# Performance work log

Measured on AMD Instinct MI355X. Metric: run time of the kernel, lower is better.

The kernel has to match this reference:

```python
import jax, jax.numpy as jnp
import numpy as np

NUM_HEADS = 16
ROPE_BASE = 10000.0


def _rope_tables(head_dim, seq_len, dtype=jnp.float32):
    # Half-split convention: rotate first half against second half.
    inv_freq = 1.0 / (ROPE_BASE ** (jnp.arange(0, head_dim, 2, dtype=dtype) / head_dim))
    pos = jnp.arange(seq_len, dtype=dtype)
    angles_half = jnp.einsum('s,d->sd', pos, inv_freq)          # (S, D/2)
    angles = jnp.concatenate([angles_half, angles_half], -1)     # (S, D)
    return jnp.cos(angles), jnp.sin(angles)


def _apply_rope(x, cos, sin):
    # x: (H, S, D); cos/sin: (S, D) broadcast over heads
    half = x.shape[-1] // 2
    x1, x2 = x[..., :half], x[..., half:]
    x_rot = jnp.concatenate([-x2, x1], axis=-1)
    return x * cos + x_rot * sin


def setup_inputs() -> dict:
    key = jax.random.key(0)
    S, E = 2048, 2048
    ks = jax.random.split(key, 9)
    sc = 0.02
    return {
        'x': jax.random.normal(ks[0], (S, E), jnp.float32),
        'Wq': jax.random.normal(ks[1], (E, E), jnp.float32) * sc,
        'bq': jax.random.normal(ks[2], (E,), jnp.float32) * sc,
        'Wk': jax.random.normal(ks[3], (E, E), jnp.float32) * sc,
        'bk': jax.random.normal(ks[4], (E,), jnp.float32) * sc,
        'Wv': jax.random.normal(ks[5], (E, E), jnp.float32) * sc,
        'bv': jax.random.normal(ks[6], (E,), jnp.float32) * sc,
        'Wo': jax.random.normal(ks[7], (E, E), jnp.float32) * sc,
        'bo': jax.random.normal(ks[8], (E,), jnp.float32) * sc,
    }


def reference(x, Wq, bq, Wk, bk, Wv, bv, Wo, bo):
    S, E = x.shape
    H = NUM_HEADS
    D = E // H
    scale = D ** 0.5
    cos, sin = _rope_tables(D, S, x.dtype)

    def proj(W, b):
        return (x @ W.T + b).reshape(S, H, D).transpose(1, 0, 2)  # (H, S, D)

    q = _apply_rope(proj(Wq, bq), cos, sin)
    k = _apply_rope(proj(Wk, bk), cos, sin)
    v = proj(Wv, bv)

    scores = jnp.einsum('hsd,htd->hst', q, k) / scale  # (H, S, S)
    attn = jax.nn.softmax(scores, axis=-1)
    out = jnp.einsum('hst,htd->hsd', attn, v)          # (H, S, D)
    # Faithful to the original's transpose(0,1).view(S,E) on a (1,H,S,D)
    # tensor: an in-order (head-major) flatten reinterpreted as (S, E).
    out = out.reshape(S, E)
    return out @ Wo.T + bo
```

## Files before the change

### kernel.cpp

```cpp
#include <hip/hip_runtime.h>

#define SDIM 2048
#define EDIM 2048
#define NHEAD 16
#define DHEAD 128

typedef __attribute__((ext_vector_type(8))) short short8;
typedef __attribute__((ext_vector_type(4))) float floatx4;

__device__ __forceinline__ float bf2f(ushort u) {
    union { uint i; float f; } v; v.i = ((uint)u) << 16; return v.f;
}
__device__ __forceinline__ ushort f2bf(float f) {
    union { float f; uint i; } v; v.f = f;
    uint r = v.i + 0x7fff + ((v.i >> 16) & 1);
    return (ushort)(r >> 16);
}

__device__ __forceinline__ void gload_lds16(const ushort* g, ushort* l) {
    __builtin_amdgcn_global_load_lds(
        (const __attribute__((address_space(1))) void*)g,
        (__attribute__((address_space(3))) void*)l, 16, 0, 0);
}

__global__ void convert5_kernel(
    const float* __restrict__ s0, const float* __restrict__ s1,
    const float* __restrict__ s2, const float* __restrict__ s3,
    const float* __restrict__ s4,
    ushort* __restrict__ d0, ushort* __restrict__ d1,
    ushort* __restrict__ d2, ushort* __restrict__ d3,
    ushort* __restrict__ d4)
{
    const float* src; ushort* dst;
    switch (blockIdx.y) {
        case 0: src = s0; dst = d0; break;
        case 1: src = s1; dst = d1; break;
        case 2: src = s2; dst = d2; break;
        case 3: src = s3; dst = d3; break;
        default: src = s4; dst = d4; break;
    }
    int i = blockIdx.x * blockDim.x + threadIdx.x;
    float4 f = ((const float4*)src)[i];
    ushort4 o;
    o.x = f2bf(f.x); o.y = f2bf(f.y); o.z = f2bf(f.z); o.w = f2bf(f.w);
    ((ushort4*)dst)[i] = o;
}

#define QPRESCALE 0.12754245f

template <int MODE>
__global__ __launch_bounds__(512, 2) void gemm256(
    const ushort* __restrict__ A,
    const ushort* __restrict__ B0, const ushort* __restrict__ B1, const ushort* __restrict__ B2,
    const float* __restrict__ s0, const float* __restrict__ s1, const float* __restrict__ s2,
    ushort* __restrict__ C0, ushort* __restrict__ C1, ushort* __restrict__ Vtg,
    float* __restrict__ Cf)
{
    __shared__ __align__(16) ushort smem[2][2][2][128 * 64];

    const int tid  = threadIdx.x;
    const int lane = tid & 63;
    const int wave = tid >> 6;
    const int l15 = lane & 15, quad = lane >> 4, l7 = lane & 7;
    const int wm = wave & 1, wn = wave >> 1;
    const int bm = blockIdx.x * 256;

    int which = 0, ks = 0, n0, NT;
    const ushort* Abase;
    const ushort* Bsel;
    const float*  bia;
    if constexpr (MODE == 0) {
        which = blockIdx.y >> 3;
        n0 = (blockIdx.y & 7) * 256;
        NT = EDIM / 64;
        Abase = A;
        Bsel = (which == 0) ? B0 : (which == 1) ? B1 : B2;
        bia  = (which == 0) ? s0 : (which == 1) ? s1 : s2;
    } else {
        ks = blockIdx.y >> 3;
        n0 = (blockIdx.y & 7) * 256;
        NT = (EDIM / 2) / 64;
        Abase = A + ks * (EDIM / 2);
        Bsel  = B0 + ks * (EDIM / 2);
        bia   = s0;
    }

    const int srow = tid >> 3;
    const int sgc  = (((tid & 7) ^ ((tid >> 3) & 7)) << 3);

    floatx4 acc[8][4];
#pragma unroll
    for (int i = 0; i < 8; i++)
#pragma unroll
        for (int j = 0; j < 4; j++) acc[i][j] = (floatx4)0.0f;

    auto stageA = [&](int tile, int h) {
        const ushort* g = Abase + (size_t)(bm + h * 128 + srow) * EDIM + tile * 64 + sgc;
        ushort* l = &smem[tile & 1][0][h][0] + tid * 8;
        gload_lds16(g, l);
        gload_lds16(g + (size_t)64 * EDIM, l + 4096);
    };
    auto stageB = [&](int tile, int h) {
        const ushort* g = Bsel + (size_t)(n0 + h * 128 + srow) * EDIM + tile * 64 + sgc;
        ushort* l = &smem[tile & 1][1][h][0] + tid * 8;
        gload_lds16(g, l);
        gload_lds16(g + (size_t)64 * EDIM, l + 4096);
    };

    stageA(0, 0); stageA(0, 1); stageB(0, 0); stageB(0, 1);
    stageB(1, 0); stageB(1, 1);
    asm volatile("s_waitcnt vmcnt(4)" ::: "memory");
    __builtin_amdgcn_s_barrier();

    const int c0 = ((quad ^ l7) << 3);
    const int c1 = (((quad + 4) ^ l7) << 3);
    const int brow0 = (wn & 1) * 64;

    short8 af[4], b0[4], b1[4];

#define MFMA16(AOFF, AF, BF) \
    _Pragma("unroll") \
    for (int mf = 0; mf < 4; mf++) \
        _Pragma("unroll") \
        for (int an = 0; an < 4; an++) \
            acc[(AOFF) + mf][an] = __builtin_amdgcn_mfma_f32_16x16x32_bf16( \
                AF[mf], BF[an], acc[(AOFF) + mf][an], 0, 0, 0);

#define PH_PRE() do { \
    asm volatile("" ::: "memory"); \
    __builtin_amdgcn_s_barrier(); \
    asm volatile("s_waitcnt lgkmcnt(0)" ::: "memory"); \
    __builtin_amdgcn_sched_barrier(0); \
    __builtin_amdgcn_s_setprio(1); \
} while (0)
#define PH_POST() do { \
    __builtin_amdgcn_s_setprio(0); \
    asm volatile("" ::: "memory"); \
    __builtin_amdgcn_s_barrier(); \
} while (0)

    for (int t = 0; t < NT; ++t) {
        const ushort* aH = &smem[t & 1][0][wm][0];
        const ushort* bH = &smem[t & 1][1][wn >> 1][0];

#pragma unroll
        for (int mf = 0; mf < 4; mf++)
            af[mf] = *(const short8*)(aH + (mf * 16 + l15) * 64 + c0);
#pragma unroll
        for (int an = 0; an < 4; an++)
            b0[an] = *(const short8*)(bH + (brow0 + an * 16 + l15) * 64 + c0);
        if (t + 1 < NT) stageA(t + 1, 0);
        PH_PRE();
        MFMA16(0, af, b0);
        PH_POST();

        short8 ag[4];
#pragma unroll
        for (int mf = 0; mf < 4; mf++)
            ag[mf] = *(const short8*)(aH + (mf * 16 + l15) * 64 + c1);
#pragma unroll
        for (int an = 0; an < 4; an++)
            b1[an] = *(const short8*)(bH + (brow0 + an * 16 + l15) * 64 + c1);
        if (t + 1 < NT) stageA(t + 1, 1);
        PH_PRE();
        MFMA16(0, ag, b1);
        PH_POST();

#pragma unroll
        for (int mf = 0; mf < 4; mf++)
            af[mf] = *(const short8*)(aH + (64 + mf * 16 + l15) * 64 + c0);
        if (t + 2 < NT) stageB(t + 2, 0);
        PH_PRE();
        MFMA16(4, af, b0);
        PH_POST();

#pragma unroll
        for (int mf = 0; mf < 4; mf++)
            ag[mf] = *(const short8*)(aH + (64 + mf * 16 + l15) * 64 + c1);
        if (t + 2 < NT) stageB(t + 2, 1);
        asm volatile("" ::: "memory");
        __builtin_amdgcn_s_barrier();
        asm volatile("s_waitcnt lgkmcnt(0)" ::: "memory");
        __builtin_amdgcn_sched_barrier(0);
        __builtin_amdgcn_s_setprio(1);
        MFMA16(4, ag, b1);
        __builtin_amdgcn_s_setprio(0);
        if (t < NT - 2) asm volatile("s_waitcnt vmcnt(4)" ::: "memory");
        else            asm volatile("s_waitcnt vmcnt(0)" ::: "memory");
        __builtin_amdgcn_s_barrier();
    }
#undef MFMA16
#undef PH_PRE
#undef PH_POST

    if constexpr (MODE == 1) {
#pragma unroll
        for (int an = 0; an < 4; an++) {
            int col = n0 + wn * 64 + an * 16 + l15;
            float bv = (ks == 0) ? bia[col] : 0.0f;
#pragma unroll
            for (int am = 0; am < 8; am++) {
                int row = bm + wm * 128 + am * 16 + quad * 4;
#pragma unroll
                for (int r = 0; r < 4; r++)
                    atomicAdd(&Cf[(size_t)(row + r) * EDIM + col], acc[am][an][r] + bv);
            }
        }
        return;
    }

    if (which == 2) {
#pragma unroll
        for (int an = 0; an < 4; an++) {
            int col = n0 + wn * 64 + an * 16 + l15;
            int h = col >> 7, d = col & 127;
            float bv = bia[col];
            ushort* cp = Vtg + (size_t)h * SDIM * DHEAD + (size_t)d * SDIM;
#pragma unroll
            for (int am = 0; am < 8; am++) {
                int s = bm + wm * 128 + am * 16 + quad * 4;
                ushort4 pk;
                pk.x = f2bf(acc[am][an][0] + bv);
                pk.y = f2bf(acc[am][an][1] + bv);
                pk.z = f2bf(acc[am][an][2] + bv);
                pk.w = f2bf(acc[am][an][3] + bv);
                *(ushort4*)(cp + s) = pk;
            }
        }
    } else {
        ushort* C = (which == 0) ? C0 : C1;
        const float psc = (which == 0) ? QPRESCALE : 1.0f;
        float* xch = (float*)smem;
        float bv[4], invf[4];
#pragma unroll
        for (int an = 0; an < 4; an++) {
            bv[an]   = bia[n0 + wn * 64 + an * 16 + l15];
            invf[an] = __expf((float)(an * 16 + l15) * -0.14391157f);
        }
        const int mybase = wave * 1024 + quad * 16 + l15;
        const int pbase  = (wave ^ 2) * 1024 + quad * 16 + l15;
        const int rowb = bm + wm * 128 + quad * 4;
#pragma unroll
        for (int am2 = 0; am2 < 4; am2++) {
            __syncthreads();
#pragma unroll
            for (int sl = 0; sl < 2; sl++) {
                int am = am2 * 2 + sl;
#pragma unroll
                for (int an = 0; an < 4; an++)
#pragma unroll
                    for (int r = 0; r < 4; r++)
                        xch[sl * 8192 + mybase + an * 256 + r * 64] = acc[am][an][r] + bv[an];
            }
            __syncthreads();
#pragma unroll
            for (int sl = 0; sl < 2; sl++) {
                int am = am2 * 2 + sl;
#pragma unroll
                for (int an = 0; an < 4; an++) {
                    int col = n0 + wn * 64 + an * 16 + l15;
#pragma unroll
                    for (int r = 0; r < 4; r++) {
                        int row = rowb + am * 16 + r;
                        float v = acc[am][an][r] + bv[an];
                        float w = xch[sl * 8192 + pbase + an * 256 + r * 64];
                        float ang = (float)row * invf[an];
                        float rev = ang * 0.15915494309f;
                        rev -= floorf(rev);
                        float arad = rev * 6.28318530718f;
                        float sn = __sinf(arad), cs = __cosf(arad);
                        float o = ((wn & 1) == 0) ? (v * cs - w * sn) : (v * cs + w * sn);
                        C[(size_t)row * EDIM + col] = f2bf(o * psc);
                    }
                }
            }
        }
    }
}

template <typename OUTT, int KSPLIT>
__global__ __launch_bounds__(256) void gemm_bt(
    const ushort* __restrict__ A,
    const ushort* __restrict__ B0, const ushort* __restrict__ B1, const ushort* __restrict__ B2,
    const float* __restrict__ s0, const float* __restrict__ s1, const float* __restrict__ s2,
    OUTT* __restrict__ C0, OUTT* __restrict__ C1, OUTT* __restrict__ C2,
    int nbpm)
{
    __shared__ __align__(16) ushort smem[2 * 128 * 32];
    ushort* a_s = smem;
    ushort* b_s = smem + 128 * 32;

    const int tid = threadIdx.x;
    const int wave = tid >> 6, lane = tid & 63;
    const int l15 = lane & 15, quad = lane >> 4;
    const int wm = wave & 1, wn = wave >> 1;
    const int bm = blockIdx.x * 128;
    const int which = blockIdx.y / nbpm;
    const int n0 = (blockIdx.y % nbpm) * 128;

    const ushort* B;
    const float*  bia;
    OUTT*         C;
    const ushort* Abase;
    if constexpr (KSPLIT == 2) {
        B = B0; bia = s0; C = C0;
        Abase = A + which * (EDIM / 2);
    } else {
        B   = (which == 0) ? B0 : (which == 1) ? B1 : B2;
        bia = (which == 0) ? s0 : (which == 1) ? s1 : s2;
        C   = (which == 0) ? C0 : (which == 1) ? C1 : C2;
        Abase = A;
    }
    const ushort* Bbase = (KSPLIT == 2) ? B + which * (EDIM / 2) : B;

    floatx4 acc[4][4];
#pragma unroll
    for (int i = 0; i < 4; i++)
#pragma unroll
        for (int j = 0; j < 4; j++) acc[i][j] = (floatx4)0.0f;

    const int t1 = tid + 256;
    const int row0 = tid >> 2, kc0 = (tid & 3) * 8;
    const int row1 = t1 >> 2,  kc1 = (t1 & 3) * 8;

    for (int k0 = 0; k0 < EDIM / KSPLIT; k0 += 32) {
        __syncthreads();
        gload_lds16(Abase + (size_t)(bm + row0) * EDIM + k0 + kc0, a_s + tid * 8);
        gload_lds16(Abase + (size_t)(bm + row1) * EDIM + k0 + kc1, a_s + t1 * 8);
        gload_lds16(Bbase + (size_t)(n0 + row0) * EDIM + k0 + kc0, b_s + tid * 8);
        gload_lds16(Bbase + (size_t)(n0 + row1) * EDIM + k0 + kc1, b_s + t1 * 8);
        __syncthreads();

        short8 af[4], bf[4];
#pragma unroll
        for (int mt = 0; mt < 4; mt++)
            af[mt] = *(const short8*)(a_s + (wm * 64 + mt * 16 + l15) * 32 + quad * 8);
#pragma unroll
        for (int nt = 0; nt < 4; nt++)
            bf[nt] = *(const short8*)(b_s + (wn * 64 + nt * 16 + l15) * 32 + quad * 8);
#pragma unroll
        for (int mt = 0; mt < 4; mt++)
#pragma unroll
            for (int nt = 0; nt < 4; nt++)
                acc[mt][nt] = __builtin_amdgcn_mfma_f32_16x16x32_bf16(af[mt], bf[nt], acc[mt][nt], 0, 0, 0);
    }

    if constexpr (KSPLIT == 2) {
#pragma unroll
        for (int nt = 0; nt < 4; nt++) {
            int col = n0 + wn * 64 + nt * 16 + l15;
            float bv = (which == 0) ? bia[col] : 0.0f;
#pragma unroll
            for (int mt = 0; mt < 4; mt++) {
#pragma unroll
                for (int r = 0; r < 4; r++) {
                    int row = bm + wm * 64 + mt * 16 + quad * 4 + r;
                    atomicAdd(&((float*)C)[(size_t)row * EDIM + col], acc[mt][nt][r] + bv);
                }
            }
        }
    } else {
#pragma unroll
        for (int nt = 0; nt < 4; nt++) {
            int col = n0 + wn * 64 + nt * 16 + l15;
            float bv = bia[col];
#pragma unroll
            for (int mt = 0; mt < 4; mt++) {
#pragma unroll
                for (int r = 0; r < 4; r++) {
                    int row = bm + wm * 64 + mt * 16 + quad * 4 + r;
                    float v = acc[mt][nt][r] + bv;
                    if constexpr (sizeof(OUTT) == 2)
                        ((ushort*)C)[(size_t)row * EDIM + col] = f2bf(v);
                    else
                        ((float*)C)[(size_t)row * EDIM + col] = v;
                }
            }
        }
    }
}

#define MFIX2 17.31234049f
__global__ __launch_bounds__(256, 4) void attn_kernel(
    const ushort* __restrict__ Q, const ushort* __restrict__ K,
    const ushort* __restrict__ Vtg,
    ushort* __restrict__ Opart, float* __restrict__ Lsum,
    ushort* __restrict__ Ab, int nsplit)
{
    __shared__ __align__(16) ushort Ks[64 * 128];
    __shared__ __align__(16) ushort Vt[128 * 64];
    __shared__ __align__(16) ushort Ps[64 * 64];

    const int bid = blockIdx.x;
    const int head = bid & 15, qt = (bid >> 4) & 31, half = bid >> 9;
    const int tid = threadIdx.x, wave = tid >> 6, lane = tid & 63;
    const int l15 = lane & 15, quad = lane >> 4;
    const int l7 = l15 & 7;
    const int kstart = half * (SDIM / nsplit);
    const int ntile = (SDIM / nsplit) / 64;

    short8 qf[4];
    {
        int s = qt * 64 + wave * 16 + l15;
        const ushort* qp = Q + (size_t)s * EDIM + head * DHEAD;
#pragma unroll
        for (int kc = 0; kc < 4; kc++) qf[kc] = *(const short8*)(qp + kc * 32 + quad * 8);
    }

    floatx4 o[8];
#pragma unroll
    for (int i = 0; i < 8; i++) o[i] = (floatx4)0.0f;
    float lsum = 0.0f;

    const int krow = tid >> 4, kc8 = tid & 15;
    const int vd = tid >> 3, vc8 = tid & 7;
    const int prow = wave * 16 + l15;

    for (int kv = 0; kv < ntile; kv++) {
        const int k0 = kstart + kv * 64;
        __syncthreads();
#pragma unroll
        for (int i = 0; i < 4; i++) {
            int row = krow + i * 16;
            uint4 v = *(const uint4*)(K + (size_t)(k0 + row) * EDIM + head * DHEAD + kc8 * 8);
            *(uint4*)(Ks + row * 128 + ((kc8 ^ (row & 7)) << 3)) = v;
        }
#pragma unroll
        for (int i = 0; i < 4; i++) {
            int d = vd + i * 32;
            uint4 v = *(const uint4*)(Vtg + (size_t)head * SDIM * DHEAD + (size_t)d * SDIM + k0 + vc8 * 8);
            *(uint4*)(Vt + d * 64 + ((vc8 ^ (d & 7)) << 3)) = v;
        }
        __syncthreads();

#pragma unroll
        for (int nt = 0; nt < 4; nt++) {
            floatx4 st = (floatx4)0.0f;
#pragma unroll
            for (int kc = 0; kc < 4; kc++) {
                short8 kfr = *(const short8*)(Ks + (nt * 16 + l15) * 128 + (((kc * 4 + quad) ^ l7) << 3));
                st = __builtin_amdgcn_mfma_f32_16x16x32_bf16(kfr, qf[kc], st, 0, 0, 0);
            }
            ushort4 pk;
            float p0 = __builtin_amdgcn_exp2f(st[0] - MFIX2);
            float p1 = __builtin_amdgcn_exp2f(st[1] - MFIX2);
            float p2 = __builtin_amdgcn_exp2f(st[2] - MFIX2);
            float p3 = __builtin_amdgcn_exp2f(st[3] - MFIX2);
            lsum += (p0 + p1) + (p2 + p3);
            pk.x = f2bf(p0); pk.y = f2bf(p1); pk.z = f2bf(p2); pk.w = f2bf(p3);
            int c2 = (nt * 2 + (quad >> 1)) ^ l7;
            *(ushort4*)(Ps + prow * 64 + (c2 << 3) + ((quad & 1) << 2)) = pk;
        }

#pragma unroll
        for (int kc2 = 0; kc2 < 2; kc2++) {
            short8 af = *(const short8*)(Ps + prow * 64 + (((kc2 * 4 + quad) ^ l7) << 3));
#pragma unroll
            for (int nt2 = 0; nt2 < 8; nt2++) {
                short8 bfr = *(const short8*)(Vt + (nt2 * 16 + l15) * 64 + (((kc2 * 4 + quad) ^ l7) << 3));
                o[nt2] = __builtin_amdgcn_mfma_f32_16x16x32_bf16(af, bfr, o[nt2], 0, 0, 0);
            }
        }
    }

    lsum += __shfl_xor(lsum, 16);
    lsum += __shfl_xor(lsum, 32);

    if (nsplit == 1) {
        float invl[4];
#pragma unroll
        for (int r = 0; r < 4; r++) invl[r] = 1.0f / __shfl(lsum, quad * 4 + r, 16);
#pragma unroll
        for (int nt2 = 0; nt2 < 8; nt2++) {
#pragma unroll
            for (int r = 0; r < 4; r++) {
                int s = qt * 64 + wave * 16 + quad * 4 + r;
                int d = nt2 * 16 + l15;
                Ab[(size_t)head * SDIM * DHEAD + (size_t)s * DHEAD + d] = f2bf(o[nt2][r] * invl[r]);
            }
        }
    } else {
        size_t pb = ((size_t)half * NHEAD + head) * SDIM * DHEAD;
#pragma unroll
        for (int nt2 = 0; nt2 < 8; nt2++) {
#pragma unroll
            for (int r = 0; r < 4; r++) {
                int s = qt * 64 + wave * 16 + quad * 4 + r;
                int d = nt2 * 16 + l15;
                Opart[pb + (size_t)s * DHEAD + d] = f2bf(o[nt2][r]);
            }
        }
        if (lane < 16)
            Lsum[((size_t)half * NHEAD + head) * SDIM + qt * 64 + wave * 16 + lane] = lsum;
    }
}

__global__ void merge_kernel(const ushort* __restrict__ Opart,
                             const float* __restrict__ Lsum,
                             ushort* __restrict__ Ab)
{
    const int HS = NHEAD * SDIM;
    int t = blockIdx.x * blockDim.x + threadIdx.x;
    int row = t >> 4, c8 = (t & 15) * 8;
    float inv = 1.0f / (Lsum[row] + Lsum[HS + row] + Lsum[2 * HS + row] + Lsum[3 * HS + row]);
    float acc[8] = {0, 0, 0, 0, 0, 0, 0, 0};
#pragma unroll
    for (int p = 0; p < 4; p++) {
        union { uint4 v; ushort u[8]; } a;
        a.v = *(const uint4*)(Opart + (size_t)p * HS * DHEAD + (size_t)row * DHEAD + c8);
#pragma unroll
        for (int j = 0; j < 8; j++) acc[j] += bf2f(a.u[j]);
    }
    union { uint4 v; ushort u[8]; } ro;
#pragma unroll
    for (int j = 0; j < 8; j++) ro.u[j] = f2bf(acc[j] * inv);
    *(uint4*)(Ab + (size_t)row * DHEAD + c8) = ro.v;
}

extern "C" void kernel_launch(void* const* d_in, const int* in_sizes, int n_in,
                              void* d_out, int out_size, void* d_ws, size_t ws_size,
                              hipStream_t stream) {
    (void)in_sizes; (void)n_in; (void)out_size;
    const float* x  = (const float*)d_in[0];
    const float* Wq = (const float*)d_in[1];
    const float* bq = (const float*)d_in[2];
    const float* Wk = (const float*)d_in[3];
    const float* bk = (const float*)d_in[4];
    const float* Wv = (const float*)d_in[5];
    const float* bv = (const float*)d_in[6];
    const float* Wo = (const float*)d_in[7];
    const float* bo = (const float*)d_in[8];
    float* out = (float*)d_out;

    char* ws = (char*)d_ws;
    const size_t SEG = (size_t)EDIM * EDIM * 2;
    ushort* xb  = (ushort*)(ws + 0 * SEG);
    ushort* Wqb = (ushort*)(ws + 1 * SEG);
    ushort* Wkb = (ushort*)(ws + 2 * SEG);
    ushort* Wvb = (ushort*)(ws + 3 * SEG);
    ushort* Wob = (ushort*)(ws + 4 * SEG);
    ushort* Qb  = (ushort*)(ws + 5 * SEG);
    ushort* Kb  = (ushort*)(ws + 6 * SEG);
    ushort* Vtg = (ushort*)(ws + 7 * SEG);
    ushort* Ab  = (ushort*)(ws + 8 * SEG);
    ushort* Op  = (ushort*)(ws + 0 * SEG);
    float*  Ls  = (float*)(ws + 11 * SEG);

    const int split = (ws_size >= ((size_t)89 << 20)) ? 1 : 0;

    convert5_kernel<<<dim3(4096, 5), 256, 0, stream>>>(
        x, Wq, Wk, Wv, Wo, xb, Wqb, Wkb, Wvb, Wob);

    gemm256<0><<<dim3(8, 24), 512, 0, stream>>>(
        xb, Wqb, Wkb, Wvb, bq, bk, bv, Qb, Kb, Vtg, nullptr);

    if (split) {
        attn_kernel<<<2048, 256, 0, stream>>>(Qb, Kb, Vtg, Op, Ls, Ab, 4);
        merge_kernel<<<2048, 256, 0, stream>>>(Op, Ls, Ab);
        hipMemsetAsync(out, 0, (size_t)EDIM * EDIM * 4, stream);
        gemm256<1><<<dim3(8, 16), 512, 0, stream>>>(
            Ab, Wob, nullptr, nullptr, bo, nullptr, nullptr,
            nullptr, nullptr, nullptr, out);
    } else {
        attn_kernel<<<512, 256, 0, stream>>>(Qb, Kb, Vtg, Op, Ls, Ab, 1);
        gemm_bt<float, 1><<<dim3(16, 16), 256, 0, stream>>>(
            Ab, Wob, Wob, Wob, bo, bo, bo, out, out, out, 16);
    }
}
```

Measured before the change: 299.9 us.

## Specialize QKV GEMM, merge last two MFMA phases, prioritize attention MFMAs

```diff
diff --git a/kernel.cpp b/kernel.cpp
--- a/kernel.cpp
+++ b/kernel.cpp
@@ -48,13 +48,11 @@
 
 #define QPRESCALE 0.12754245f
 
-template <int MODE>
-__global__ __launch_bounds__(512, 2) void gemm256(
+__global__ __launch_bounds__(512, 2) void gemm256_qkv(
     const ushort* __restrict__ A,
     const ushort* __restrict__ B0, const ushort* __restrict__ B1, const ushort* __restrict__ B2,
     const float* __restrict__ s0, const float* __restrict__ s1, const float* __restrict__ s2,
-    ushort* __restrict__ C0, ushort* __restrict__ C1, ushort* __restrict__ Vtg,
-    float* __restrict__ Cf)
+    ushort* __restrict__ C0, ushort* __restrict__ C1, ushort* __restrict__ Vtg)
 {
     __shared__ __align__(16) ushort smem[2][2][2][128 * 64];
 
@@ -64,26 +62,12 @@
     const int l15 = lane & 15, quad = lane >> 4, l7 = lane & 7;
     const int wm = wave & 1, wn = wave >> 1;
     const int bm = blockIdx.x * 256;
-
-    int which = 0, ks = 0, n0, NT;
-    const ushort* Abase;
-    const ushort* Bsel;
-    const float*  bia;
-    if constexpr (MODE == 0) {
-        which = blockIdx.y >> 3;
-        n0 = (blockIdx.y & 7) * 256;
-        NT = EDIM / 64;
-        Abase = A;
-        Bsel = (which == 0) ? B0 : (which == 1) ? B1 : B2;
-        bia  = (which == 0) ? s0 : (which == 1) ? s1 : s2;
-    } else {
-        ks = blockIdx.y >> 3;
-        n0 = (blockIdx.y & 7) * 256;
-        NT = (EDIM / 2) / 64;
-        Abase = A + ks * (EDIM / 2);
-        Bsel  = B0 + ks * (EDIM / 2);
-        bia   = s0;
-    }
+    const int which = blockIdx.y >> 3;
+    const int n0 = (blockIdx.y & 7) * 256;
+    const int NT = EDIM / 64;
+
+    const ushort* Bsel = (which == 0) ? B0 : (which == 1) ? B1 : B2;
+    const float*  bia  = (which == 0) ? s0 : (which == 1) ? s1 : s2;
 
     const int srow = tid >> 3;
     const int sgc  = (((tid & 7) ^ ((tid >> 3) & 7)) << 3);
@@ -95,7 +79,7 @@
         for (int j = 0; j < 4; j++) acc[i][j] = (floatx4)0.0f;
 
     auto stageA = [&](int tile, int h) {
-        const ushort* g = Abase + (size_t)(bm + h * 128 + srow) * EDIM + tile * 64 + sgc;
+        const ushort* g = A + (size_t)(bm + h * 128 + srow) * EDIM + tile * 64 + sgc;
         ushort* l = &smem[tile & 1][0][h][0] + tid * 8;
         gload_lds16(g, l);
         gload_lds16(g + (size_t)64 * EDIM, l + 4096);
@@ -116,7 +100,7 @@
     const int c1 = (((quad + 4) ^ l7) << 3);
     const int brow0 = (wn & 1) * 64;
 
-    short8 af[4], b0[4], b1[4];
+    short8 a0[4], a1[4], b0[4], b1[4];
 
 #define MFMA16(AOFF, AF, BF) \
     _Pragma("unroll") \
@@ -145,45 +129,40 @@
 
 #pragma unroll
         for (int mf = 0; mf < 4; mf++)
-            af[mf] = *(const short8*)(aH + (mf * 16 + l15) * 64 + c0);
+            a0[mf] = *(const short8*)(aH + (mf * 16 + l15) * 64 + c0);
 #pragma unroll
         for (int an = 0; an < 4; an++)
             b0[an] = *(const short8*)(bH + (brow0 + an * 16 + l15) * 64 + c0);
         if (t + 1 < NT) stageA(t + 1, 0);
         PH_PRE();
-        MFMA16(0, af, b0);
+        MFMA16(0, a0, b0);
         PH_POST();
 
-        short8 ag[4];
 #pragma unroll
         for (int mf = 0; mf < 4; mf++)
-            ag[mf] = *(const short8*)(aH + (mf * 16 + l15) * 64 + c1);
+            a1[mf] = *(const short8*)(aH + (mf * 16 + l15) * 64 + c1);
 #pragma unroll
         for (int an = 0; an < 4; an++)
             b1[an] = *(const short8*)(bH + (brow0 + an * 16 + l15) * 64 + c1);
         if (t + 1 < NT) stageA(t + 1, 1);
         PH_PRE();
-        MFMA16(0, ag, b1);
+        MFMA16(0, a1, b1);
         PH_POST();
 
 #pragma unroll
         for (int mf = 0; mf < 4; mf++)
-            af[mf] = *(const short8*)(aH + (64 + mf * 16 + l15) * 64 + c0);
-        if (t + 2 < NT) stageB(t + 2, 0);
-        PH_PRE();
-        MFMA16(4, af, b0);
-        PH_POST();
-
+            a0[mf] = *(const short8*)(aH + (64 + mf * 16 + l15) * 64 + c0);
 #pragma unroll
         for (int mf = 0; mf < 4; mf++)
-            ag[mf] = *(const short8*)(aH + (64 + mf * 16 + l15) * 64 + c1);
-        if (t + 2 < NT) stageB(t + 2, 1);
+            a1[mf] = *(const short8*)(aH + (64 + mf * 16 + l15) * 64 + c1);
+        if (t + 2 < NT) { stageB(t + 2, 0); stageB(t + 2, 1); }
         asm volatile("" ::: "memory");
         __builtin_amdgcn_s_barrier();
         asm volatile("s_waitcnt lgkmcnt(0)" ::: "memory");
         __builtin_amdgcn_sched_barrier(0);
         __builtin_amdgcn_s_setprio(1);
-        MFMA16(4, ag, b1);
+        MFMA16(4, a0, b0);
+        MFMA16(4, a1, b1);
         __builtin_amdgcn_s_setprio(0);
         if (t < NT - 2) asm volatile("s_waitcnt vmcnt(4)" ::: "memory");
         else            asm volatile("s_waitcnt vmcnt(0)" ::: "memory");
@@ -192,22 +171,6 @@
 #undef MFMA16
 #undef PH_PRE
 #undef PH_POST
-
-    if constexpr (MODE == 1) {
-#pragma unroll
-        for (int an = 0; an < 4; an++) {
-            int col = n0 + wn * 64 + an * 16 + l15;
-            float bv = (ks == 0) ? bia[col] : 0.0f;
-#pragma unroll
-            for (int am = 0; am < 8; am++) {
-                int row = bm + wm * 128 + am * 16 + quad * 4;
-#pragma unroll
-                for (int r = 0; r < 4; r++)
-                    atomicAdd(&Cf[(size_t)(row + r) * EDIM + col], acc[am][an][r] + bv);
-            }
-        }
-        return;
-    }
 
     if (which == 2) {
 #pragma unroll
@@ -436,11 +399,13 @@
 #pragma unroll
         for (int nt = 0; nt < 4; nt++) {
             floatx4 st = (floatx4)0.0f;
+            __builtin_amdgcn_s_setprio(1);
 #pragma unroll
             for (int kc = 0; kc < 4; kc++) {
                 short8 kfr = *(const short8*)(Ks + (nt * 16 + l15) * 128 + (((kc * 4 + quad) ^ l7) << 3));
                 st = __builtin_amdgcn_mfma_f32_16x16x32_bf16(kfr, qf[kc], st, 0, 0, 0);
             }
+            __builtin_amdgcn_s_setprio(0);
             ushort4 pk;
             float p0 = __builtin_amdgcn_exp2f(st[0] - MFIX2);
             float p1 = __builtin_amdgcn_exp2f(st[1] - MFIX2);
@@ -452,6 +417,7 @@
             *(ushort4*)(Ps + prow * 64 + (c2 << 3) + ((quad & 1) << 2)) = pk;
         }
 
+        __builtin_amdgcn_s_setprio(1);
 #pragma unroll
         for (int kc2 = 0; kc2 < 2; kc2++) {
             short8 af = *(const short8*)(Ps + prow * 64 + (((kc2 * 4 + quad) ^ l7) << 3));
@@ -461,6 +427,7 @@
                 o[nt2] = __builtin_amdgcn_mfma_f32_16x16x32_bf16(af, bfr, o[nt2], 0, 0, 0);
             }
         }
+        __builtin_amdgcn_s_setprio(0);
     }
 
     lsum += __shfl_xor(lsum, 16);
@@ -551,16 +518,15 @@
     convert5_kernel<<<dim3(4096, 5), 256, 0, stream>>>(
         x, Wq, Wk, Wv, Wo, xb, Wqb, Wkb, Wvb, Wob);
 
-    gemm256<0><<<dim3(8, 24), 512, 0, stream>>>(
-        xb, Wqb, Wkb, Wvb, bq, bk, bv, Qb, Kb, Vtg, nullptr);
+    gemm256_qkv<<<dim3(8, 24), 512, 0, stream>>>(
+        xb, Wqb, Wkb, Wvb, bq, bk, bv, Qb, Kb, Vtg);
 
     if (split) {
         attn_kernel<<<2048, 256, 0, stream>>>(Qb, Kb, Vtg, Op, Ls, Ab, 4);
         merge_kernel<<<2048, 256, 0, stream>>>(Op, Ls, Ab);
         hipMemsetAsync(out, 0, (size_t)EDIM * EDIM * 4, stream);
-        gemm256<1><<<dim3(8, 16), 512, 0, stream>>>(
-            Ab, Wob, nullptr, nullptr, bo, nullptr, nullptr,
-            nullptr, nullptr, nullptr, out);
+        gemm_bt<float, 2><<<dim3(16, 32), 256, 0, stream>>>(
+            Ab, Wob, Wob, Wob, bo, bo, bo, out, out, out, 16);
     } else {
         attn_kernel<<<512, 256, 0, stream>>>(Qb, Kb, Vtg, Op, Ls, Ab, 1);
         gemm_bt<float, 1><<<dim3(16, 16), 256, 0, stream>>>(
```

Result: no change. 297.4 us (-0.8%).
